# Performance work log

Measured on AMD Instinct MI355X. Metric: run time of the kernel, lower is better.

Reference implementation:

```python
import jax, jax.numpy as jnp
import numpy as np

D_MODEL = 1024
HEADS = 16
D_K = D_MODEL // HEADS
B, S = 2, 2048


def setup_inputs() -> dict:
    key = jax.random.key(0)
    ks = jax.random.split(key, 11)
    sc = 1.0 / np.sqrt(D_MODEL)
    return {
        "q": jax.random.normal(ks[0], (B, S, D_MODEL), jnp.float32),
        "k": jax.random.normal(ks[1], (B, S, D_MODEL), jnp.float32),
        "v": jax.random.normal(ks[2], (B, S, D_MODEL), jnp.float32),
        "Wq": jax.random.normal(ks[3], (D_MODEL, D_MODEL), jnp.float32) * sc,
        "bq": jnp.zeros((D_MODEL,), jnp.float32),
        "Wk": jax.random.normal(ks[4], (D_MODEL, D_MODEL), jnp.float32) * sc,
        "bk": jnp.zeros((D_MODEL,), jnp.float32),
        "Wv": jax.random.normal(ks[5], (D_MODEL, D_MODEL), jnp.float32) * sc,
        "bv": jnp.zeros((D_MODEL,), jnp.float32),
        "Wo": jax.random.normal(ks[6], (D_MODEL, D_MODEL), jnp.float32) * sc,
        "bo": jnp.zeros((D_MODEL,), jnp.float32),
    }


def reference(q, k, v, Wq, bq, Wk, bk, Wv, bv, Wo, bo):
    bs = q.shape[0]
    # linear projections then split heads: [B,S,D] -> [B,H,S,Dk]
    def proj(x, W, b):
        y = x @ W.T + b
        return y.reshape(bs, -1, HEADS, D_K).transpose(0, 2, 1, 3)

    qh = proj(q, Wq, bq)
    kh = proj(k, Wk, bk)
    vh = proj(v, Wv, bv)
    # scores: [B,H,Sq,Sk] -- full attention matrix as in the original
    scores = jnp.einsum("bhqd,bhkd->bhqk", qh, kh) / jnp.sqrt(
        jnp.asarray(D_K, jnp.float32))
    attn = jax.nn.softmax(scores, axis=-1)
    # dropout is identity in eval/reference mode
    out = jnp.einsum("bhqk,bhkd->bhqd", attn, vh)
    concat = out.transpose(0, 2, 1, 3).reshape(bs, -1, D_MODEL)
    return concat @ Wo.T + bo
```

## Files before the change

### kernel.cpp

```cpp
#include <hip/hip_runtime.h>
#include <hip/hip_bf16.h>

typedef __attribute__((ext_vector_type(8))) short bf16x8;
typedef __attribute__((ext_vector_type(4))) float f32x4;
typedef __attribute__((ext_vector_type(16))) float f32x16;

#define DM   1024
#define SEQ  2048
#define NB   2
#define NH   16
#define MR   (NB*SEQ)

#define SMK  (MR*DM)
#define W1M  (DM*DM)

#define QSCALE 0.18033688011112042f

#define OFF_QB  ((size_t)0)
#define OFF_KB  ((size_t)SMK)
#define OFF_VB  ((size_t)(2*(size_t)SMK))
#define OFF_WQ  ((size_t)(3*(size_t)SMK))
#define OFF_WO  ((size_t)(3*(size_t)SMK + 3*(size_t)W1M))
#define OFF_QP  ((size_t)(3*(size_t)SMK + 4*(size_t)W1M))
#define OFF_KP  ((size_t)(4*(size_t)SMK + 4*(size_t)W1M))
#define OFF_VP  ((size_t)(5*(size_t)SMK + 4*(size_t)W1M))
#define OFF_CC  ((size_t)0)

__device__ __forceinline__ unsigned short f2bf(float f) {
  union { __hip_bfloat16 b; unsigned short u; } cv;
  cv.b = __float2bfloat16(f);
  return cv.u;
}

__device__ __forceinline__ unsigned int cvtpk_bf16(float lo, float hi) {
  unsigned int r;
  asm("v_cvt_pk_bf16_f32 %0, %1, %2" : "=v"(r) : "v"(lo), "v"(hi));
  return r;
}

__device__ __forceinline__ void plane32_swap(unsigned int& a, unsigned int& b) {
  asm("v_permlane32_swap_b32 %0, %1" : "+v"(a), "+v"(b));
}

__global__ __launch_bounds__(256) void cvt_all(const float* __restrict__ q,
                                               const float* __restrict__ k,
                                               const float* __restrict__ v,
                                               const float* __restrict__ wq,
                                               const float* __restrict__ wk,
                                               const float* __restrict__ wv,
                                               const float* __restrict__ wo,
                                               unsigned short* __restrict__ ws) {
  int i = blockIdx.x * 256 + threadIdx.x;
  const float* src;
  unsigned short* dst;
  int j;
  if (i < 3 * (SMK / 4)) {
    int z = i >> 20;
    j = i & ((SMK / 4) - 1);
    src = (z == 0) ? q : ((z == 1) ? k : v);
    dst = ws + OFF_QB + (size_t)z * SMK;
  } else {
    int i2 = i - 3 * (SMK / 4);
    int z = i2 >> 18;
    j = i2 & ((W1M / 4) - 1);
    src = (z == 0) ? wq : ((z == 1) ? wk : ((z == 2) ? wv : wo));
    dst = ws + OFF_WQ + (size_t)z * W1M;
  }
  float4 val = reinterpret_cast<const float4*>(src)[j];
  ushort4 o;
  o.x = f2bf(val.x); o.y = f2bf(val.y); o.z = f2bf(val.z); o.w = f2bf(val.w);
  reinterpret_cast<ushort4*>(dst)[j] = o;
}

__device__ __forceinline__ void gload_lds16(const void* g, void* l) {
  __builtin_amdgcn_global_load_lds(
      (const __attribute__((address_space(1))) unsigned int*)g,
      (__attribute__((address_space(3))) unsigned int*)l,
      16, 0, 0);
}

template<int BM, int BN, bool OUT_BF16, bool BIAS_ROW>
__device__ __forceinline__ void gemm_bt_body(unsigned short* __restrict__ As,
                                             unsigned short* __restrict__ Bs,
                                             const unsigned short* __restrict__ A,
                                             const unsigned short* __restrict__ Bt,
                                             const float* __restrict__ bias,
                                             void* __restrict__ Cv,
                                             int N, int K, float scale,
                                             int brow, int bcol) {
  constexpr int MREP = BM / 32;
  constexpr int NREP = BN / 32;
  constexpr int LPS  = BM / 64 + BN / 64;
  const int tid  = threadIdx.x;
  const int lane = tid & 63;
  const int w    = tid >> 6;
  const int wr   = w >> 1, wc = w & 1;

  f32x4 acc[MREP][NREP];
#pragma unroll
  for (int m = 0; m < MREP; m++)
#pragma unroll
    for (int n = 0; n < NREP; n++) acc[m][n] = (f32x4){0.f, 0.f, 0.f, 0.f};

  const int srow = lane >> 2;
  const int scol = (lane & 3) * 8;

  auto stage = [&](int buf, int k0) {
#pragma unroll
    for (int c = w; c < BM / 16; c += 4)
      gload_lds16(A + (size_t)(brow + c * 16 + srow) * K + k0 + scol,
                  (char*)As + (size_t)buf * BM * 64 + c * 1024);
#pragma unroll
    for (int c = w; c < BN / 16; c += 4)
      gload_lds16(Bt + (size_t)(bcol + c * 16 + srow) * K + k0 + scol,
                  (char*)Bs + (size_t)buf * BN * 64 + c * 1024);
  };

  stage(0, 0);
  stage(1, 32);

  const int nk = K / 32;
  const int lrow_a = wr * (BM / 2) + (lane & 15);
  const int lrow_b = wc * (BN / 2) + (lane & 15);
  const int lcol   = (lane >> 4) * 8;

  int b0 = 0;
  for (int kt = 0; kt < nk; ++kt) {
    if (kt + 1 < nk) {
      if constexpr (LPS == 4) asm volatile("s_waitcnt vmcnt(4)" ::: "memory");
      else                    asm volatile("s_waitcnt vmcnt(3)" ::: "memory");
    } else {
      asm volatile("s_waitcnt vmcnt(0)" ::: "memory");
    }
    __builtin_amdgcn_s_barrier();
    __builtin_amdgcn_sched_barrier(0);
    if (kt + 2 < nk) {
      int bn = b0 + 2; if (bn >= 3) bn -= 3;
      stage(bn, (kt + 2) * 32);
    }
    bf16x8 a[MREP], b[NREP];
#pragma unroll
    for (int m = 0; m < MREP; m++)
      a[m] = *(const bf16x8*)&As[(size_t)b0 * BM * 32 + (lrow_a + m * 16) * 32 + lcol];
#pragma unroll
    for (int n = 0; n < NREP; n++)
      b[n] = *(const bf16x8*)&Bs[(size_t)b0 * BN * 32 + (lrow_b + n * 16) * 32 + lcol];
    __builtin_amdgcn_s_setprio(1);
#pragma unroll
    for (int m = 0; m < MREP; m++)
#pragma unroll
      for (int n = 0; n < NREP; n++)
        acc[m][n] = __builtin_amdgcn_mfma_f32_16x16x32_bf16(a[m], b[n], acc[m][n], 0, 0, 0);
    __builtin_amdgcn_s_setprio(0);
    b0 = (b0 == 2) ? 0 : b0 + 1;
  }

  const int crow0 = brow + wr * (BM / 2);
  const int ccol0 = bcol + wc * (BN / 2);
  const int rsub  = (lane >> 4) * 4;
  const int csub  = lane & 15;
#pragma unroll
  for (int m = 0; m < MREP; m++)
#pragma unroll
    for (int n = 0; n < NREP; n++) {
      int col = ccol0 + n * 16 + csub;
      float bcol_v = BIAS_ROW ? 0.f : bias[col];
#pragma unroll
      for (int qq = 0; qq < 4; qq++) {
        int row = crow0 + m * 16 + rsub + qq;
        float bb = BIAS_ROW ? bias[row] : bcol_v;
        float v = (acc[m][n][qq] + bb) * scale;
        if (OUT_BF16)
          ((unsigned short*)Cv)[(size_t)row * N + col] = f2bf(v);
        else
          ((float*)Cv)[(size_t)row * N + col] = v;
      }
    }
}

__global__ __launch_bounds__(256) void gemm_qkv(unsigned short* ws,
                                                const float* __restrict__ bq,
                                                const float* __restrict__ bk,
                                                const float* __restrict__ bv) {
  __shared__ unsigned short As[3 * 128 * 32];
  __shared__ unsigned short Bs[3 * 128 * 32];
  const int i  = blockIdx.x;
  const int x  = i & 7;
  const int r  = i >> 3;
  const int pm = r >> 3;
  const int bx = r & 7;
  const int p  = x * 12 + pm;
  const int z  = p >> 5;
  const int by = p & 31;
  if (z < 2) {
    gemm_bt_body<128, 128, true, false>(
        As, Bs,
        ws + OFF_QB + (size_t)z * SMK, ws + OFF_WQ + (size_t)z * W1M,
        z ? bk : bq, ws + OFF_QP + (size_t)z * SMK,
        DM, DM, z ? 1.f : QSCALE, by * 128, bx * 128);
  } else {
    gemm_bt_body<128, 128, true, true>(
        As, Bs,
        ws + OFF_WQ + 2 * W1M, ws + OFF_VB,
        bv, ws + OFF_VP,
        MR, DM, 1.f, bx * 128, by * 128);
  }
}

__global__ __launch_bounds__(256) void gemm_out(const unsigned short* __restrict__ ws,
                                                const float* __restrict__ bo,
                                                float* __restrict__ out) {
  __shared__ unsigned short As[3 * 64 * 32];
  __shared__ unsigned short Bs[3 * 128 * 32];
  const int i  = blockIdx.x;
  const int x  = i & 7;
  const int r  = i >> 3;
  const int pm = r >> 3;
  const int bx = r & 7;
  const int by = x * 8 + pm;
  gemm_bt_body<64, 128, false, false>(
      As, Bs,
      ws + OFF_CC, ws + OFF_WO, bo, out,
      DM, DM, 1.f, by * 64, bx * 128);
}

__global__ __launch_bounds__(512, 4) void flash_attn(unsigned short* ws) {
  __shared__ __align__(16) unsigned char smem[65536];

  const int tid  = threadIdx.x;
  const int lane = tid & 63;
  const int w    = tid >> 6;
  const int s    = w >> 2;
  const int wsub = w & 3;
  const int q    = lane & 31;
  const int hi   = lane >> 5;
  const int swq  = q & 7;
  const int bid  = blockIdx.x;
  const int swzb = (bid & 7) * 64 + (bid >> 3);
  const int qblk = swzb & 15;
  const int bh   = swzb >> 4;
  const int b    = bh >> 4, h = bh & 15;

  const unsigned short* Qp = ws + OFF_QP;
  const unsigned short* Kp = ws + OFF_KP;
  const unsigned short* Vp = ws + OFF_VP;
  unsigned short* CC = ws + OFF_CC;

  const unsigned short* Kg = Kp + (size_t)(b * SEQ) * DM + h * 64;
  const unsigned short* Vg = Vp + (size_t)(h * 64) * MR + (size_t)b * SEQ;

  bf16x8 bqf[4];
  {
    const unsigned short* qrow =
        Qp + (size_t)(b * SEQ + qblk * 128 + wsub * 32 + q) * DM + h * 64;
#pragma unroll
    for (int c = 0; c < 4; c++)
      bqf[c] = *(const bf16x8*)(qrow + c * 16 + hi * 8);
  }

  f32x16 o_acc[2];
#pragma unroll
  for (int dt = 0; dt < 2; dt++)
#pragma unroll
    for (int r = 0; r < 16; r++) o_acc[dt][r] = 0.f;
  float l_run = 0.f;

  auto stage = [&](int buf, int t) {
    const unsigned short* Kt = Kg + (size_t)(s * 16 + t) * 64 * DM;
    const unsigned short* Vt = Vg + (s * 16 + t) * 64;
    char* base = (char*)smem + (size_t)(s * 2 + buf) * 16384;
#pragma unroll
    for (int i = 0; i < 2; i++) {
      int slot = wsub * 128 + i * 64 + lane;
      int srow = slot >> 3;
      int gch  = (slot & 7) ^ (srow & 7);
      gload_lds16(Kt + (size_t)srow * DM + gch * 8, base + slot * 16);
      gload_lds16(Vt + (size_t)srow * MR + gch * 8, base + 8192 + slot * 16);
    }
  };

  stage(0, 0);

  for (int t = 0; t < 16; ++t) {
    int buf = t & 1;
    __syncthreads();
    if (t + 1 < 16) stage(buf ^ 1, t + 1);
    const unsigned short* Kb = (const unsigned short*)(smem + (size_t)(s * 2 + buf) * 16384);
    const unsigned short* Vb = Kb + 4096;

    f32x16 st0, st1;
#pragma unroll
    for (int r = 0; r < 16; r++) { st0[r] = 0.f; st1[r] = 0.f; }
    __builtin_amdgcn_s_setprio(1);
#pragma unroll
    for (int c = 0; c < 4; c++) {
      int ch = (((c << 1) | hi) ^ swq) << 3;
      bf16x8 ak0 = *(const bf16x8*)&Kb[q * 64 + ch];
      bf16x8 ak1 = *(const bf16x8*)&Kb[(32 + q) * 64 + ch];
      st0 = __builtin_amdgcn_mfma_f32_32x32x16_bf16(ak0, bqf[c], st0, 0, 0, 0);
      st1 = __builtin_amdgcn_mfma_f32_32x32x16_bf16(ak1, bqf[c], st1, 0, 0, 0);
    }
    __builtin_amdgcn_s_setprio(0);

    unsigned int pk0[8], pk1[8];
    float lt = 0.f;
#pragma unroll
    for (int p = 0; p < 8; p++) {
      float a0 = __builtin_amdgcn_exp2f(st0[2 * p]);
      float a1 = __builtin_amdgcn_exp2f(st0[2 * p + 1]);
      float b0 = __builtin_amdgcn_exp2f(st1[2 * p]);
      float b1 = __builtin_amdgcn_exp2f(st1[2 * p + 1]);
      lt += (a0 + a1) + (b0 + b1);
      pk0[p] = cvtpk_bf16(a0, a1);
      pk1[p] = cvtpk_bf16(b0, b1);
    }
    l_run += lt;

    plane32_swap(pk0[0], pk0[2]); plane32_swap(pk0[1], pk0[3]);
    plane32_swap(pk0[4], pk0[6]); plane32_swap(pk0[5], pk0[7]);
    plane32_swap(pk1[0], pk1[2]); plane32_swap(pk1[1], pk1[3]);
    plane32_swap(pk1[4], pk1[6]); plane32_swap(pk1[5], pk1[7]);

    __builtin_amdgcn_s_setprio(1);
#pragma unroll
    for (int t4 = 0; t4 < 4; t4++) {
      union { unsigned int u[4]; bf16x8 v; } pb;
      const unsigned int* src = (t4 < 2) ? pk0 : pk1;
      pb.u[0] = src[(t4 & 1) * 4 + 0];
      pb.u[1] = src[(t4 & 1) * 4 + 1];
      pb.u[2] = src[(t4 & 1) * 4 + 2];
      pb.u[3] = src[(t4 & 1) * 4 + 3];
      int ch = (((t4 << 1) | hi) ^ swq) << 3;
#pragma unroll
      for (int dt = 0; dt < 2; dt++) {
        bf16x8 av = *(const bf16x8*)&Vb[(dt * 32 + q) * 64 + ch];
        o_acc[dt] = __builtin_amdgcn_mfma_f32_32x32x16_bf16(av, pb.v, o_acc[dt], 0, 0, 0);
      }
    }
    __builtin_amdgcn_s_setprio(0);
  }

  __syncthreads();
  float* scr = (float*)smem;
  float lsum = l_run + __shfl_xor(l_run, 32, 64);
  if (s == 1) {
    int idx = (wsub * 64 + lane) * 33;
#pragma unroll
    for (int dt = 0; dt < 2; dt++)
#pragma unroll
      for (int r = 0; r < 16; r++) scr[idx + dt * 16 + r] = o_acc[dt][r];
    scr[idx + 32] = lsum;
  }
  __syncthreads();
  if (s == 0) {
    int idx = (wsub * 64 + lane) * 33;
#pragma unroll
    for (int dt = 0; dt < 2; dt++)
#pragma unroll
      for (int r = 0; r < 16; r++) o_acc[dt][r] += scr[idx + dt * 16 + r];
    float l = lsum + scr[idx + 32];
    float inv = 1.f / l;

    int qg = b * SEQ + qblk * 128 + wsub * 32 + q;
    unsigned short* crow = CC + (size_t)qg * DM + h * 64;
#pragma unroll
    for (int dt = 0; dt < 2; dt++)
#pragma unroll
      for (int rq = 0; rq < 4; rq++) {
        ushort4 o;
        o.x = f2bf(o_acc[dt][4 * rq + 0] * inv);
        o.y = f2bf(o_acc[dt][4 * rq + 1] * inv);
        o.z = f2bf(o_acc[dt][4 * rq + 2] * inv);
        o.w = f2bf(o_acc[dt][4 * rq + 3] * inv);
        *(ushort4*)&crow[dt * 32 + rq * 8 + hi * 4] = o;
      }
  }
}

extern "C" void kernel_launch(void* const* d_in, const int* in_sizes, int n_in,
                              void* d_out, int out_size, void* d_ws, size_t ws_size,
                              hipStream_t stream) {
  const float* q  = (const float*)d_in[0];
  const float* k  = (const float*)d_in[1];
  const float* v  = (const float*)d_in[2];
  const float* Wq = (const float*)d_in[3];
  const float* bq = (const float*)d_in[4];
  const float* Wk = (const float*)d_in[5];
  const float* bk = (const float*)d_in[6];
  const float* Wv = (const float*)d_in[7];
  const float* bv = (const float*)d_in[8];
  const float* Wo = (const float*)d_in[9];
  const float* bo = (const float*)d_in[10];

  unsigned short* ws = (unsigned short*)d_ws;
  float* out = (float*)d_out;

  cvt_all<<<dim3((3 * (SMK / 4) + 4 * (W1M / 4)) / 256), dim3(256), 0, stream>>>(
      q, k, v, Wq, Wk, Wv, Wo, ws);

  gemm_qkv<<<dim3(768), dim3(256), 0, stream>>>(ws, bq, bk, bv);

  flash_attn<<<dim3(512), dim3(512), 0, stream>>>(ws);

  gemm_out<<<dim3(512), dim3(256), 0, stream>>>(ws, bo, out);
}
```

Before: 116.6 us.

## Fuse fp32-to-bf16 conversion of inputs and QKV weights into the QKV GEMM

Drops the standalone conversion pass over q/k/v and Wq/Wk/Wv. The QKV GEMM now loads fp32 tiles into registers, packs them to bf16 with v_cvt_pk_bf16_f32, and stores them to a double-buffered LDS ring. Only Wo is still pre-converted, and the output GEMM gets its own specialised body. This removes a full read-write pass over about 50MB of fp32 data, but the GEMM now reads fp32 (twice the bytes per tile) and loses the async global-to-LDS path and one pipeline stage.

```diff
diff --git a/kernel.cpp b/kernel.cpp
--- a/kernel.cpp
+++ b/kernel.cpp
@@ -17,9 +17,6 @@
 #define QSCALE 0.18033688011112042f
 
 #define OFF_QB  ((size_t)0)
-#define OFF_KB  ((size_t)SMK)
-#define OFF_VB  ((size_t)(2*(size_t)SMK))
-#define OFF_WQ  ((size_t)(3*(size_t)SMK))
 #define OFF_WO  ((size_t)(3*(size_t)SMK + 3*(size_t)W1M))
 #define OFF_QP  ((size_t)(3*(size_t)SMK + 4*(size_t)W1M))
 #define OFF_KP  ((size_t)(4*(size_t)SMK + 4*(size_t)W1M))
@@ -42,34 +39,13 @@
   asm("v_permlane32_swap_b32 %0, %1" : "+v"(a), "+v"(b));
 }
 
-__global__ __launch_bounds__(256) void cvt_all(const float* __restrict__ q,
-                                               const float* __restrict__ k,
-                                               const float* __restrict__ v,
-                                               const float* __restrict__ wq,
-                                               const float* __restrict__ wk,
-                                               const float* __restrict__ wv,
-                                               const float* __restrict__ wo,
-                                               unsigned short* __restrict__ ws) {
+__global__ __launch_bounds__(256) void cvt_wo(const float* __restrict__ wo,
+                                              unsigned short* __restrict__ dst) {
   int i = blockIdx.x * 256 + threadIdx.x;
-  const float* src;
-  unsigned short* dst;
-  int j;
-  if (i < 3 * (SMK / 4)) {
-    int z = i >> 20;
-    j = i & ((SMK / 4) - 1);
-    src = (z == 0) ? q : ((z == 1) ? k : v);
-    dst = ws + OFF_QB + (size_t)z * SMK;
-  } else {
-    int i2 = i - 3 * (SMK / 4);
-    int z = i2 >> 18;
-    j = i2 & ((W1M / 4) - 1);
-    src = (z == 0) ? wq : ((z == 1) ? wk : ((z == 2) ? wv : wo));
-    dst = ws + OFF_WQ + (size_t)z * W1M;
-  }
-  float4 val = reinterpret_cast<const float4*>(src)[j];
+  float4 v = reinterpret_cast<const float4*>(wo)[i];
   ushort4 o;
-  o.x = f2bf(val.x); o.y = f2bf(val.y); o.z = f2bf(val.z); o.w = f2bf(val.w);
-  reinterpret_cast<ushort4*>(dst)[j] = o;
+  o.x = f2bf(v.x); o.y = f2bf(v.y); o.z = f2bf(v.z); o.w = f2bf(v.w);
+  reinterpret_cast<ushort4*>(dst)[i] = o;
 }
 
 __device__ __forceinline__ void gload_lds16(const void* g, void* l) {
@@ -79,111 +55,121 @@
       16, 0, 0);
 }
 
-template<int BM, int BN, bool OUT_BF16, bool BIAS_ROW>
-__device__ __forceinline__ void gemm_bt_body(unsigned short* __restrict__ As,
-                                             unsigned short* __restrict__ Bs,
-                                             const unsigned short* __restrict__ A,
-                                             const unsigned short* __restrict__ Bt,
-                                             const float* __restrict__ bias,
-                                             void* __restrict__ Cv,
-                                             int N, int K, float scale,
-                                             int brow, int bcol) {
-  constexpr int MREP = BM / 32;
-  constexpr int NREP = BN / 32;
-  constexpr int LPS  = BM / 64 + BN / 64;
+template<bool BIAS_ROW>
+__device__ __forceinline__ void gemm_f32_body(unsigned short* __restrict__ As,
+                                              unsigned short* __restrict__ Bs,
+                                              const float* __restrict__ A,
+                                              const float* __restrict__ B,
+                                              const float* __restrict__ bias,
+                                              unsigned short* __restrict__ C,
+                                              int N, int K, float scale,
+                                              int brow, int bcol) {
   const int tid  = threadIdx.x;
   const int lane = tid & 63;
   const int w    = tid >> 6;
   const int wr   = w >> 1, wc = w & 1;
 
-  f32x4 acc[MREP][NREP];
-#pragma unroll
-  for (int m = 0; m < MREP; m++)
-#pragma unroll
-    for (int n = 0; n < NREP; n++) acc[m][n] = (f32x4){0.f, 0.f, 0.f, 0.f};
+  f32x4 acc[4][4];
+#pragma unroll
+  for (int m = 0; m < 4; m++)
+#pragma unroll
+    for (int n = 0; n < 4; n++) acc[m][n] = (f32x4){0.f, 0.f, 0.f, 0.f};
 
   const int srow = lane >> 2;
   const int scol = (lane & 3) * 8;
 
-  auto stage = [&](int buf, int k0) {
-#pragma unroll
-    for (int c = w; c < BM / 16; c += 4)
-      gload_lds16(A + (size_t)(brow + c * 16 + srow) * K + k0 + scol,
-                  (char*)As + (size_t)buf * BM * 64 + c * 1024);
-#pragma unroll
-    for (int c = w; c < BN / 16; c += 4)
-      gload_lds16(Bt + (size_t)(bcol + c * 16 + srow) * K + k0 + scol,
-                  (char*)Bs + (size_t)buf * BN * 64 + c * 1024);
+  f32x4 fa[2][2], fb[2][2];
+
+  auto loadst = [&](int k0) {
+#pragma unroll
+    for (int i = 0; i < 2; i++) {
+      const float* pa = A + (size_t)(brow + (w + i * 4) * 16 + srow) * K + k0 + scol;
+      fa[i][0] = *(const f32x4*)pa;
+      fa[i][1] = *(const f32x4*)(pa + 4);
+      const float* pb = B + (size_t)(bcol + (w + i * 4) * 16 + srow) * K + k0 + scol;
+      fb[i][0] = *(const f32x4*)pb;
+      fb[i][1] = *(const f32x4*)(pb + 4);
+    }
   };
-
-  stage(0, 0);
-  stage(1, 32);
+  auto commit = [&](int buf) {
+#pragma unroll
+    for (int i = 0; i < 2; i++) {
+      union { unsigned int u[4]; bf16x8 v8; } ua, ub;
+#pragma unroll
+      for (int j = 0; j < 2; j++) {
+        ua.u[2 * j]     = cvtpk_bf16(fa[i][j][0], fa[i][j][1]);
+        ua.u[2 * j + 1] = cvtpk_bf16(fa[i][j][2], fa[i][j][3]);
+        ub.u[2 * j]     = cvtpk_bf16(fb[i][j][0], fb[i][j][1]);
+        ub.u[2 * j + 1] = cvtpk_bf16(fb[i][j][2], fb[i][j][3]);
+      }
+      *(bf16x8*)((char*)As + (size_t)buf * 8192 + (w + i * 4) * 1024 + lane * 16) = ua.v8;
+      *(bf16x8*)((char*)Bs + (size_t)buf * 8192 + (w + i * 4) * 1024 + lane * 16) = ub.v8;
+    }
+  };
+
+  loadst(0);
+  commit(0);
+  loadst(32);
 
   const int nk = K / 32;
-  const int lrow_a = wr * (BM / 2) + (lane & 15);
-  const int lrow_b = wc * (BN / 2) + (lane & 15);
+  const int lrow_a = wr * 64 + (lane & 15);
+  const int lrow_b = wc * 64 + (lane & 15);
   const int lcol   = (lane >> 4) * 8;
 
-  int b0 = 0;
   for (int kt = 0; kt < nk; ++kt) {
-    if (kt + 1 < nk) {
-      if constexpr (LPS == 4) asm volatile("s_waitcnt vmcnt(4)" ::: "memory");
-      else                    asm volatile("s_waitcnt vmcnt(3)" ::: "memory");
-    } else {
-      asm volatile("s_waitcnt vmcnt(0)" ::: "memory");
-    }
+    int buf = kt & 1;
+    asm volatile("s_waitcnt lgkmcnt(0)" ::: "memory");
     __builtin_amdgcn_s_barrier();
     __builtin_amdgcn_sched_barrier(0);
-    if (kt + 2 < nk) {
-      int bn = b0 + 2; if (bn >= 3) bn -= 3;
-      stage(bn, (kt + 2) * 32);
-    }
-    bf16x8 a[MREP], b[NREP];
-#pragma unroll
-    for (int m = 0; m < MREP; m++)
-      a[m] = *(const bf16x8*)&As[(size_t)b0 * BM * 32 + (lrow_a + m * 16) * 32 + lcol];
-#pragma unroll
-    for (int n = 0; n < NREP; n++)
-      b[n] = *(const bf16x8*)&Bs[(size_t)b0 * BN * 32 + (lrow_b + n * 16) * 32 + lcol];
+    if (kt + 1 < nk) commit(buf ^ 1);
+    if (kt + 2 < nk) loadst((kt + 2) * 32);
+    bf16x8 a[4], b[4];
+#pragma unroll
+    for (int m = 0; m < 4; m++)
+      a[m] = *(const bf16x8*)&As[(size_t)buf * 4096 + (lrow_a + m * 16) * 32 + lcol];
+#pragma unroll
+    for (int n = 0; n < 4; n++)
+      b[n] = *(const bf16x8*)&Bs[(size_t)buf * 4096 + (lrow_b + n * 16) * 32 + lcol];
     __builtin_amdgcn_s_setprio(1);
 #pragma unroll
-    for (int m = 0; m < MREP; m++)
-#pragma unroll
-      for (int n = 0; n < NREP; n++)
+    for (int m = 0; m < 4; m++)
+#pragma unroll
+      for (int n = 0; n < 4; n++)
         acc[m][n] = __builtin_amdgcn_mfma_f32_16x16x32_bf16(a[m], b[n], acc[m][n], 0, 0, 0);
     __builtin_amdgcn_s_setprio(0);
-    b0 = (b0 == 2) ? 0 : b0 + 1;
-  }
-
-  const int crow0 = brow + wr * (BM / 2);
-  const int ccol0 = bcol + wc * (BN / 2);
+  }
+
+  const int crow0 = brow + wr * 64;
+  const int ccol0 = bcol + wc * 64;
   const int rsub  = (lane >> 4) * 4;
   const int csub  = lane & 15;
 #pragma unroll
-  for (int m = 0; m < MREP; m++)
-#pragma unroll
-    for (int n = 0; n < NREP; n++) {
+  for (int m = 0; m < 4; m++)
+#pragma unroll
+    for (int n = 0; n < 4; n++) {
       int col = ccol0 + n * 16 + csub;
       float bcol_v = BIAS_ROW ? 0.f : bias[col];
 #pragma unroll
       for (int qq = 0; qq < 4; qq++) {
         int row = crow0 + m * 16 + rsub + qq;
         float bb = BIAS_ROW ? bias[row] : bcol_v;
-        float v = (acc[m][n][qq] + bb) * scale;
-        if (OUT_BF16)
-          ((unsigned short*)Cv)[(size_t)row * N + col] = f2bf(v);
-        else
-          ((float*)Cv)[(size_t)row * N + col] = v;
+        C[(size_t)row * N + col] = f2bf((acc[m][n][qq] + bb) * scale);
       }
     }
 }
 
-__global__ __launch_bounds__(256) void gemm_qkv(unsigned short* ws,
-                                                const float* __restrict__ bq,
-                                                const float* __restrict__ bk,
-                                                const float* __restrict__ bv) {
-  __shared__ unsigned short As[3 * 128 * 32];
-  __shared__ unsigned short Bs[3 * 128 * 32];
+__global__ __launch_bounds__(256, 3) void gemm_qkv(const float* __restrict__ q,
+                                                   const float* __restrict__ k,
+                                                   const float* __restrict__ v,
+                                                   const float* __restrict__ Wq,
+                                                   const float* __restrict__ Wk,
+                                                   const float* __restrict__ Wv,
+                                                   unsigned short* ws,
+                                                   const float* __restrict__ bq,
+                                                   const float* __restrict__ bk,
+                                                   const float* __restrict__ bv) {
+  __shared__ unsigned short As[2 * 128 * 32];
+  __shared__ unsigned short Bs[2 * 128 * 32];
   const int i  = blockIdx.x;
   const int x  = i & 7;
   const int r  = i >> 3;
@@ -193,18 +179,103 @@
   const int z  = p >> 5;
   const int by = p & 31;
   if (z < 2) {
-    gemm_bt_body<128, 128, true, false>(
-        As, Bs,
-        ws + OFF_QB + (size_t)z * SMK, ws + OFF_WQ + (size_t)z * W1M,
-        z ? bk : bq, ws + OFF_QP + (size_t)z * SMK,
-        DM, DM, z ? 1.f : QSCALE, by * 128, bx * 128);
+    gemm_f32_body<false>(As, Bs,
+                         z ? k : q, z ? Wk : Wq, z ? bk : bq,
+                         ws + OFF_QP + (size_t)z * SMK,
+                         DM, DM, z ? 1.f : QSCALE, by * 128, bx * 128);
   } else {
-    gemm_bt_body<128, 128, true, true>(
-        As, Bs,
-        ws + OFF_WQ + 2 * W1M, ws + OFF_VB,
-        bv, ws + OFF_VP,
-        MR, DM, 1.f, bx * 128, by * 128);
-  }
+    gemm_f32_body<true>(As, Bs,
+                        Wv, v, bv,
+                        ws + OFF_VP,
+                        MR, DM, 1.f, bx * 128, by * 128);
+  }
+}
+
+__device__ __forceinline__ void gemm_out_body(unsigned short* __restrict__ As,
+                                              unsigned short* __restrict__ Bs,
+                                              const unsigned short* __restrict__ A,
+                                              const unsigned short* __restrict__ Bt,
+                                              const float* __restrict__ bias,
+                                              float* __restrict__ Cv,
+                                              int N, int K,
+                                              int brow, int bcol) {
+  constexpr int BM = 64, BN = 128;
+  const int tid  = threadIdx.x;
+  const int lane = tid & 63;
+  const int w    = tid >> 6;
+  const int wr   = w >> 1, wc = w & 1;
+
+  f32x4 acc[2][4];
+#pragma unroll
+  for (int m = 0; m < 2; m++)
+#pragma unroll
+    for (int n = 0; n < 4; n++) acc[m][n] = (f32x4){0.f, 0.f, 0.f, 0.f};
+
+  const int srow = lane >> 2;
+  const int scol = (lane & 3) * 8;
+
+  auto stage = [&](int buf, int k0) {
+#pragma unroll
+    for (int c = w; c < BM / 16; c += 4)
+      gload_lds16(A + (size_t)(brow + c * 16 + srow) * K + k0 + scol,
+                  (char*)As + (size_t)buf * BM * 64 + c * 1024);
+#pragma unroll
+    for (int c = w; c < BN / 16; c += 4)
+      gload_lds16(Bt + (size_t)(bcol + c * 16 + srow) * K + k0 + scol,
+                  (char*)Bs + (size_t)buf * BN * 64 + c * 1024);
+  };
+
+  stage(0, 0);
+  stage(1, 32);
+
+  const int nk = K / 32;
+  const int lrow_a = wr * (BM / 2) + (lane & 15);
+  const int lrow_b = wc * (BN / 2) + (lane & 15);
+  const int lcol   = (lane >> 4) * 8;
+
+  int b0 = 0;
+  for (int kt = 0; kt < nk; ++kt) {
+    if (kt + 1 < nk) asm volatile("s_waitcnt vmcnt(3)" ::: "memory");
+    else             asm volatile("s_waitcnt vmcnt(0)" ::: "memory");
+    __builtin_amdgcn_s_barrier();
+    __builtin_amdgcn_sched_barrier(0);
+    if (kt + 2 < nk) {
+      int bn = b0 + 2; if (bn >= 3) bn -= 3;
+      stage(bn, (kt + 2) * 32);
+    }
+    bf16x8 a[2], b[4];
+#pragma unroll
+    for (int m = 0; m < 2; m++)
+      a[m] = *(const bf16x8*)&As[(size_t)b0 * BM * 32 + (lrow_a + m * 16) * 32 + lcol];
+#pragma unroll
+    for (int n = 0; n < 4; n++)
+      b[n] = *(const bf16x8*)&Bs[(size_t)b0 * BN * 32 + (lrow_b + n * 16) * 32 + lcol];
+    __builtin_amdgcn_s_setprio(1);
+#pragma unroll
+    for (int m = 0; m < 2; m++)
+#pragma unroll
+      for (int n = 0; n < 4; n++)
+        acc[m][n] = __builtin_amdgcn_mfma_f32_16x16x32_bf16(a[m], b[n], acc[m][n], 0, 0, 0);
+    __builtin_amdgcn_s_setprio(0);
+    b0 = (b0 == 2) ? 0 : b0 + 1;
+  }
+
+  const int crow0 = brow + wr * (BM / 2);
+  const int ccol0 = bcol + wc * (BN / 2);
+  const int rsub  = (lane >> 4) * 4;
+  const int csub  = lane & 15;
+#pragma unroll
+  for (int m = 0; m < 2; m++)
+#pragma unroll
+    for (int n = 0; n < 4; n++) {
+      int col = ccol0 + n * 16 + csub;
+      float bv = bias[col];
+#pragma unroll
+      for (int qq = 0; qq < 4; qq++) {
+        int row = crow0 + m * 16 + rsub + qq;
+        Cv[(size_t)row * N + col] = acc[m][n][qq] + bv;
+      }
+    }
 }
 
 __global__ __launch_bounds__(256) void gemm_out(const unsigned short* __restrict__ ws,
@@ -218,10 +289,9 @@
   const int pm = r >> 3;
   const int bx = r & 7;
   const int by = x * 8 + pm;
-  gemm_bt_body<64, 128, false, false>(
-      As, Bs,
-      ws + OFF_CC, ws + OFF_WO, bo, out,
-      DM, DM, 1.f, by * 64, bx * 128);
+  gemm_out_body(As, Bs,
+                ws + OFF_CC, ws + OFF_WO, bo, out,
+                DM, DM, by * 64, bx * 128);
 }
 
 __global__ __launch_bounds__(512, 4) void flash_attn(unsigned short* ws) {
@@ -395,10 +465,9 @@
   unsigned short* ws = (unsigned short*)d_ws;
   float* out = (float*)d_out;
 
-  cvt_all<<<dim3((3 * (SMK / 4) + 4 * (W1M / 4)) / 256), dim3(256), 0, stream>>>(
-      q, k, v, Wq, Wk, Wv, Wo, ws);
-
-  gemm_qkv<<<dim3(768), dim3(256), 0, stream>>>(ws, bq, bk, bv);
+  cvt_wo<<<dim3((W1M / 4) / 256), dim3(256), 0, stream>>>(Wo, ws + OFF_WO);
+
+  gemm_qkv<<<dim3(768), dim3(256), 0, stream>>>(q, k, v, Wq, Wk, Wv, ws, bq, bk, bv);
 
   flash_attn<<<dim3(512), dim3(512), 0, stream>>>(ws);
 
```

Result: faster. 112.1 us (-3.9%).
